# Kernel optimization log

Hardware: AMD Instinct MI355X
Metric: run time of the kernel (lower is better)

Reference implementation:

```python
import jax, jax.numpy as jnp
import numpy as np

N_NODES = 100000


def setup_inputs() -> dict:
    key = jax.random.key(0)
    ks = jax.random.split(key, 6)
    F_IN, F_CH, F_OUT = 64, 64, 64
    E = 1200000
    x = jax.random.normal(ks[0], (N_NODES, F_IN), dtype=jnp.float32)
    edge_index = jax.random.randint(ks[1], (2, E), 0, N_NODES, dtype=jnp.int64)
    # MLP params (PyTorch Linear default init scale ~ 1/sqrt(fan_in))
    s1 = 1.0 / np.sqrt(2 * F_IN)
    s2 = 1.0 / np.sqrt(F_CH)
    W1 = jax.random.uniform(ks[2], (2 * F_IN, F_CH), jnp.float32, -s1, s1)
    b1 = jax.random.uniform(ks[3], (F_CH,), jnp.float32, -s1, s1)
    W2 = jax.random.uniform(ks[4], (F_CH, F_OUT), jnp.float32, -s2, s2)
    b2 = jax.random.uniform(ks[5], (F_OUT,), jnp.float32, -s2, s2)
    return {"x": x, "edge_index": edge_index, "W1": W1, "b1": b1, "W2": W2, "b2": b2}


def reference(x, edge_index, W1, b1, W2, b2):
    # PyG EdgeConv with aggr='add': out_i = sum_j MLP(concat[x_i, x_j - x_i])
    src = edge_index[0]  # j (source / neighbor)
    dst = edge_index[1]  # i (target, aggregation index)
    x_i = x[dst]                     # [E, F]
    x_j = x[src]                     # [E, F]
    msg = jnp.concatenate([x_i, x_j - x_i], axis=-1)      # [E, 2F]
    h = jax.nn.relu(msg @ W1 + b1) @ W2 + b2               # [E, F_out]
    agg = jax.ops.segment_sum(h, dst, num_segments=N_NODES)  # [N, F_out]
    return jnp.tanh(agg)
```

## Files before the change

kernel.cpp:

```cpp
#include <hip/hip_runtime.h>
#include <math.h>


#define FDIM 64
#define BN 128
#define BSH 7
#define CAPB 2048
#define MAXB 1024
#define EPB 4096
#define XS_W 33
#define PRE_SMEM 24832

typedef unsigned int u32;
typedef unsigned short u16;
typedef _Float16 hf;

__device__ __forceinline__ float bf_lo(u32 u) {
    union { u32 i; float f; } c; c.i = u << 16; return c.f;
}
__device__ __forceinline__ float bf_hi(u32 u) {
    union { u32 i; float f; } c; c.i = u & 0xffff0000u; return c.f;
}
__device__ __forceinline__ u32 f2bf_rne(float f) {
    union { float f; u32 u; } c; c.f = f;
    u32 u = c.u;
    u += 0x7fffu + ((u >> 16) & 1u);
    return u >> 16;
}
__device__ __forceinline__ u32 f2h(float f) {
    union { u16 s; hf h; } c; c.h = (hf)f; return (u32)c.s;
}
__device__ __forceinline__ float h_lo(u32 u) {
    union { u16 s; hf h; } c; c.s = (u16)(u & 0xffffu); return (float)c.h;
}
__device__ __forceinline__ float h_hi(u32 u) {
    union { u16 s; hf h; } c; c.s = (u16)(u >> 16); return (float)c.h;
}

__global__ __launch_bounds__(256) void wprep_k(
    const float* __restrict__ W1, const float* __restrict__ W2,
    u32* __restrict__ Wchg, u32* __restrict__ W2hg)
{
    const int tid = threadIdx.x;
    for (int i = tid; i < 4096; i += 256) {
        int k = i >> 6, p = i & 63;
        u32 pk;
        if (p < 32) {
            int c = p * 2;
            float a0 = W1[k * 64 + c]     - W1[(64 + k) * 64 + c];
            float a1 = W1[k * 64 + c + 1] - W1[(64 + k) * 64 + c + 1];
            pk = f2h(a0) | (f2h(a1) << 16);
        } else {
            int c = (p - 32) * 2;
            pk = f2h(W1[(64 + k) * 64 + c]) | (f2h(W1[(64 + k) * 64 + c + 1]) << 16);
        }
        Wchg[i] = pk;
    }
    for (int i = tid; i < 2048; i += 256) {
        int k = i >> 5, c2 = i & 31;
        W2hg[i] = f2h(W2[k * 64 + c2 * 2]) | (f2h(W2[k * 64 + c2 * 2 + 1]) << 16);
    }
}

__global__ __launch_bounds__(256) void prep_k(
    const float* __restrict__ x, const u32* __restrict__ Wchg,
    const float* __restrict__ b1, u16* __restrict__ Ah,
    u16* __restrict__ Bmh, const int* __restrict__ ei,
    u32* __restrict__ slotB, int* __restrict__ gcnt,
    int N, int E, int NB, int nPre, int nBin)
{
    __shared__ __align__(16) char smem[PRE_SMEM];
    const int idx = blockIdx.x;
    const int tid = threadIdx.x;

    if ((idx % 6) == 5) {
        const int bb = idx / 6;
        if (bb >= nBin) return;
        int* histL = (int*)smem;
        int* gbase = histL + MAXB;
        const int e0 = bb * EPB;

        for (int j = tid; j < NB; j += 256) histL[j] = 0;
        __syncthreads();

        #pragma unroll
        for (int i = 0; i < EPB / 256; ++i) {
            int e = e0 + i * 256 + tid;
            if (e < E) {
                int d = ei[E + e];
                atomicAdd(&histL[d >> BSH], 1);
            }
        }
        __syncthreads();

        for (int j = tid; j < NB; j += 256) {
            int h = histL[j];
            gbase[j] = (h > 0) ? atomicAdd(&gcnt[j], h) : 0;
            histL[j] = 0;
        }
        __syncthreads();

        #pragma unroll
        for (int i = 0; i < EPB / 256; ++i) {
            int e = e0 + i * 256 + tid;
            if (e < E) {
                int s = ei[e];
                int d = ei[E + e];
                int b = d >> BSH;
                int pos = gbase[b] + atomicAdd(&histL[b], 1);
                if (pos < CAPB)
                    slotB[(size_t)b * CAPB + pos] =
                        ((u32)(d & (BN - 1)) << 20) | (u32)s;
            }
        }
        return;
    }

    const int pb = idx - idx / 6;
    if (pb >= nPre) return;
    u32 (*Wch)[64] = (u32(*)[64])smem;
    u32* xs = (u32*)(smem + 16384);

    const int node0 = pb * 64;

    {
        const uint4* Wg4 = (const uint4*)Wchg;
        #pragma unroll
        for (int it = 0; it < 4; ++it) {
            int i = it * 256 + tid;
            uint4 w = Wg4[i];
            *(uint4*)&Wch[i >> 4][(i & 15) * 4] = w;
        }
    }
    {
        const float4* X4 = (const float4*)x;
        #pragma unroll
        for (int it = 0; it < 4; ++it) {
            int i = it * 256 + tid;
            int n = i >> 4, k4 = i & 15;
            int gn = node0 + n;
            float4 v = make_float4(0.f, 0.f, 0.f, 0.f);
            if (gn < N) v = X4[(size_t)gn * 16 + k4];
            xs[n * XS_W + 2 * k4]     = f2h(v.x) | (f2h(v.y) << 16);
            xs[n * XS_W + 2 * k4 + 1] = f2h(v.z) | (f2h(v.w) << 16);
        }
    }
    __syncthreads();

    const int ng = tid & 15, cg = tid >> 4;
    const int n0 = ng * 4, c0 = cg * 8;
    const int wbase = (cg & 7) * 4 + ((cg >> 3) * 32);

    float acc[4][8];
    #pragma unroll
    for (int ci = 0; ci < 8; ++ci) {
        float init = b1[(c0 + ci) & 63];
        if (c0 >= 64) init = 0.f;
        #pragma unroll
        for (int ni = 0; ni < 4; ++ni) acc[ni][ci] = init;
    }

    #pragma unroll 4
    for (int kk = 0; kk < 32; ++kk) {
        u32 xv[4];
        #pragma unroll
        for (int ni = 0; ni < 4; ++ni) xv[ni] = xs[(n0 + ni) * XS_W + kk];
        uint4 w0 = *(const uint4*)&Wch[2 * kk][wbase];
        uint4 w1 = *(const uint4*)&Wch[2 * kk + 1][wbase];
        float ws0[8] = {h_lo(w0.x), h_hi(w0.x), h_lo(w0.y), h_hi(w0.y),
                        h_lo(w0.z), h_hi(w0.z), h_lo(w0.w), h_hi(w0.w)};
        float ws1[8] = {h_lo(w1.x), h_hi(w1.x), h_lo(w1.y), h_hi(w1.y),
                        h_lo(w1.z), h_hi(w1.z), h_lo(w1.w), h_hi(w1.w)};
        #pragma unroll
        for (int ni = 0; ni < 4; ++ni) {
            float xa = h_lo(xv[ni]);
            float xb = h_hi(xv[ni]);
            #pragma unroll
            for (int ci = 0; ci < 8; ++ci)
                acc[ni][ci] += xa * ws0[ci] + xb * ws1[ci];
        }
    }

    #pragma unroll
    for (int ni = 0; ni < 4; ++ni) {
        int n = node0 + n0 + ni;
        if (n >= N) break;
        if (c0 < 64) {
            uint4 pk;
            pk.x = f2h(acc[ni][0]) | (f2h(acc[ni][1]) << 16);
            pk.y = f2h(acc[ni][2]) | (f2h(acc[ni][3]) << 16);
            pk.z = f2h(acc[ni][4]) | (f2h(acc[ni][5]) << 16);
            pk.w = f2h(acc[ni][6]) | (f2h(acc[ni][7]) << 16);
            *(uint4*)&Ah[(size_t)n * 64 + c0] = pk;
        } else {
            uint4 pk;
            pk.x = f2bf_rne(acc[ni][0]) | (f2bf_rne(acc[ni][1]) << 16);
            pk.y = f2bf_rne(acc[ni][2]) | (f2bf_rne(acc[ni][3]) << 16);
            pk.z = f2bf_rne(acc[ni][4]) | (f2bf_rne(acc[ni][5]) << 16);
            pk.w = f2bf_rne(acc[ni][6]) | (f2bf_rne(acc[ni][7]) << 16);
            *(uint4*)&Bmh[(size_t)n * 64 + (c0 - 64)] = pk;
        }
    }
}

__device__ __forceinline__ float4 relu4add(float4 acc, float4 a, float4 b) {
    acc.x += fmaxf(a.x + b.x, 0.f);
    acc.y += fmaxf(a.y + b.y, 0.f);
    acc.z += fmaxf(a.z + b.z, 0.f);
    acc.w += fmaxf(a.w + b.w, 0.f);
    return acc;
}
__device__ __forceinline__ float4 relu4add_m(float4 acc, float4 a, float4 b, bool m) {
    acc.x += m ? fmaxf(a.x + b.x, 0.f) : 0.f;
    acc.y += m ? fmaxf(a.y + b.y, 0.f) : 0.f;
    acc.z += m ? fmaxf(a.z + b.z, 0.f) : 0.f;
    acc.w += m ? fmaxf(a.w + b.w, 0.f) : 0.f;
    return acc;
}
__device__ __forceinline__ float4 bf4(uint2 u) {
    return make_float4(bf_lo(u.x), bf_hi(u.x), bf_lo(u.y), bf_hi(u.y));
}

__global__ __launch_bounds__(256) void fused_agg(
    const u16* __restrict__ Ah, const u16* __restrict__ Bmh,
    const u32* __restrict__ slotB, const int* __restrict__ gcnt,
    const u32* __restrict__ W2hg, const float* __restrict__ b2,
    float* __restrict__ out, int N)
{
    __shared__ __align__(16) u32 W2h[64][34];
    __shared__ __align__(16) u32 pool[BN * 17 * 2];
    __shared__ u32 csrS[CAPB];
    __shared__ int histL[BN];
    __shared__ int rowO[BN + 1];
    __shared__ int ofs[BN];
    __shared__ float b2s[64];

    u32* eStage = pool;
    uint2* aggTb = (uint2*)pool;

    const int tid = threadIdx.x;
    const int b = blockIdx.x;
    const int node0 = b * BN;
    const int cntB = min(gcnt[b], CAPB);

    {
        const uint4* Wg4 = (const uint4*)W2hg;
        #pragma unroll
        for (int it = 0; it < 2; ++it) {
            int i = it * 256 + tid;
            uint4 w = Wg4[i];
            *(uint4*)&W2h[i >> 3][(i & 7) * 4] = w;
        }
    }
    if (tid < 64) b2s[tid] = b2[tid];
    if (tid < BN) histL[tid] = 0;
    __syncthreads();

    for (int i = tid; i < cntB; i += 256) {
        u32 e = slotB[(size_t)b * CAPB + i];
        eStage[i] = e;
        atomicAdd(&histL[e >> 20], 1);
    }
    __syncthreads();

    if (tid < 64) {
        int l = tid;
        int h0 = histL[2 * l], h1 = histL[2 * l + 1];
        int s = h0 + h1, inc = s;
        #pragma unroll
        for (int off = 1; off < 64; off <<= 1) {
            int t = __shfl_up(inc, off);
            if (l >= off) inc += t;
        }
        int base = inc - s;
        rowO[2 * l] = base; rowO[2 * l + 1] = base + h0;
        ofs[2 * l] = base;  ofs[2 * l + 1] = base + h0;
        if (l == 63) rowO[BN] = inc;
    }
    __syncthreads();

    for (int i = tid; i < cntB; i += 256) {
        u32 e = eStage[i];
        int pos = atomicAdd(&ofs[e >> 20], 1);
        csrS[pos] = e & 0xFFFFFu;
    }
    __syncthreads();

    {
        const int q = tid & 15, ng = tid >> 4;
        const uint2* __restrict__ B2 = (const uint2*)Bmh;
        const uint2* __restrict__ A2 = (const uint2*)Ah;
        #pragma unroll
        for (int h = 0; h < 8; ++h) {
            int nl = ng + h * 16;
            int gn = node0 + nl;
            int start = rowO[nl];
            int d = (gn < N) ? (rowO[nl + 1] - start) : 0;
            float4 a = make_float4(0.f, 0.f, 0.f, 0.f);
            if (gn < N) {
                uint2 ua = A2[(size_t)gn * 16 + q];
                a = make_float4(h_lo(ua.x), h_hi(ua.x), h_lo(ua.y), h_hi(ua.y));
            }
            float4 acc = make_float4(0.f, 0.f, 0.f, 0.f);

            int j = 0;
            for (; j + 8 <= d; j += 8) {
                int ss[8];
                uint2 bb[8];
                #pragma unroll
                for (int t = 0; t < 8; ++t) ss[t] = csrS[start + j + t];
                #pragma unroll
                for (int t = 0; t < 8; ++t) bb[t] = B2[(size_t)ss[t] * 16 + q];
                #pragma unroll
                for (int t = 0; t < 8; ++t) acc = relu4add(acc, a, bf4(bb[t]));
            }
            if (j < d) {
                int ss[8];
                uint2 bb[8];
                #pragma unroll
                for (int t = 0; t < 8; ++t) ss[t] = csrS[start + min(j + t, d - 1)];
                #pragma unroll
                for (int t = 0; t < 8; ++t) bb[t] = B2[(size_t)ss[t] * 16 + q];
                acc = relu4add(acc, a, bf4(bb[0]));
                #pragma unroll
                for (int t = 1; t < 8; ++t)
                    acc = relu4add_m(acc, a, bf4(bb[t]), j + t < d);
            }
            uint2 pk;
            pk.x = f2h(acc.x) | (f2h(acc.y) << 16);
            pk.y = f2h(acc.z) | (f2h(acc.w) << 16);
            aggTb[nl * 17 + q] = pk;
        }
    }
    __syncthreads();

    {
        const int cg = tid & 15, g0 = tid >> 4;
        const int c0 = cg * 4;
        #pragma unroll
        for (int h = 0; h < 2; ++h) {
            int g = g0 + h * 16;
            int nb0 = g * 4;
            float o[4][4];
            #pragma unroll
            for (int ni = 0; ni < 4; ++ni) {
                float dg = (float)(rowO[nb0 + ni + 1] - rowO[nb0 + ni]);
                #pragma unroll
                for (int ci = 0; ci < 4; ++ci) o[ni][ci] = dg * b2s[c0 + ci];
            }
            #pragma unroll 2
            for (int kc = 0; kc < 16; ++kc) {
                uint2 u0 = aggTb[(nb0 + 0) * 17 + kc];
                uint2 u1 = aggTb[(nb0 + 1) * 17 + kc];
                uint2 u2 = aggTb[(nb0 + 2) * 17 + kc];
                uint2 u3 = aggTb[(nb0 + 3) * 17 + kc];
                #pragma unroll
                for (int kk = 0; kk < 4; ++kk) {
                    uint2 w2p = *(const uint2*)&W2h[kc * 4 + kk][cg * 2];
                    float wv[4] = {h_lo(w2p.x), h_hi(w2p.x), h_lo(w2p.y), h_hi(w2p.y)};
                    float a0 = (kk < 2) ? ((kk == 0) ? h_lo(u0.x) : h_hi(u0.x))
                                        : ((kk == 2) ? h_lo(u0.y) : h_hi(u0.y));
                    float a1 = (kk < 2) ? ((kk == 0) ? h_lo(u1.x) : h_hi(u1.x))
                                        : ((kk == 2) ? h_lo(u1.y) : h_hi(u1.y));
                    float a2 = (kk < 2) ? ((kk == 0) ? h_lo(u2.x) : h_hi(u2.x))
                                        : ((kk == 2) ? h_lo(u2.y) : h_hi(u2.y));
                    float a3 = (kk < 2) ? ((kk == 0) ? h_lo(u3.x) : h_hi(u3.x))
                                        : ((kk == 2) ? h_lo(u3.y) : h_hi(u3.y));
                    #pragma unroll
                    for (int ci = 0; ci < 4; ++ci) {
                        o[0][ci] += a0 * wv[ci];
                        o[1][ci] += a1 * wv[ci];
                        o[2][ci] += a2 * wv[ci];
                        o[3][ci] += a3 * wv[ci];
                    }
                }
            }
            #pragma unroll
            for (int ni = 0; ni < 4; ++ni) {
                int gn = node0 + nb0 + ni;
                if (gn < N) {
                    float4 r = make_float4(tanhf(o[ni][0]), tanhf(o[ni][1]),
                                           tanhf(o[ni][2]), tanhf(o[ni][3]));
                    ((float4*)out)[(size_t)gn * 16 + cg] = r;
                }
            }
        }
    }
}

extern "C" void kernel_launch(void* const* d_in, const int* in_sizes, int n_in,
                              void* d_out, int out_size, void* d_ws, size_t ws_size,
                              hipStream_t stream)
{
    const float* x  = (const float*)d_in[0];
    const int*   ei = (const int*)d_in[1];
    const float* W1 = (const float*)d_in[2];
    const float* b1 = (const float*)d_in[3];
    const float* W2 = (const float*)d_in[4];
    const float* b2 = (const float*)d_in[5];
    float* out = (float*)d_out;

    const int N = in_sizes[0] / FDIM;
    const int E = in_sizes[1] / 2;
    const int NB = (N + BN - 1) / BN;

    u16*   Ah    = (u16*)d_ws;
    u16*   Bmh   = Ah + (size_t)N * FDIM;
    u32*   slotB = (u32*)(Bmh + (size_t)N * FDIM);
    u32*   Wchg  = slotB + (size_t)NB * CAPB;
    u32*   W2hg  = Wchg + 4096;
    int*   gcnt  = (int*)(W2hg + 2048);

    hipMemsetAsync(gcnt, 0, (size_t)NB * sizeof(int), stream);

    wprep_k<<<1, 256, 0, stream>>>(W1, W2, Wchg, W2hg);

    const int nPre = (N + 63) / 64;
    const int nBin = (E + EPB - 1) / EPB;
    int T = (nPre * 6 + 4) / 5;
    while (T - T / 6 < nPre) ++T;
    if (T < 6 * nBin) T = 6 * nBin;

    prep_k<<<T, 256, 0, stream>>>(x, Wchg, b1, Ah, Bmh, ei, slotB, gcnt,
                                  N, E, NB, nPre, nBin);
    fused_agg<<<NB, 256, 0, stream>>>(Ah, Bmh, slotB, gcnt, W2hg, b2, out, N);
}
```

Before: 195.3 us.

## Fold gcnt memset into wprep, rebalance binning blocks, use packed-float ReLU accumulate

Zeroes the bin counters inside the weight-prep kernel so the separate memset launch goes away. Halves edges per binning block and changes the interleave from 1-in-6 to 1-in-4 blocks, giving more parallel binning work. Rewrites the aggregation inner loop on two-wide float vectors so the compiler can emit packed FP32 add and max. It also adds a 4-edge step and shrinks the masked tail from 8 to 4 loads to cut wasted gathers. The smaller per-block edge count means more blocks contend on the global bin-count atomics.

```diff
diff --git a/kernel.cpp b/kernel.cpp
--- a/kernel.cpp
+++ b/kernel.cpp
@@ -7,13 +7,14 @@
 #define BSH 7
 #define CAPB 2048
 #define MAXB 1024
-#define EPB 4096
+#define EPB 2048
 #define XS_W 33
 #define PRE_SMEM 24832
 
 typedef unsigned int u32;
 typedef unsigned short u16;
 typedef _Float16 hf;
+typedef float f2 __attribute__((ext_vector_type(2)));
 
 __device__ __forceinline__ float bf_lo(u32 u) {
     union { u32 i; float f; } c; c.i = u << 16; return c.f;
@@ -39,7 +40,8 @@
 
 __global__ __launch_bounds__(256) void wprep_k(
     const float* __restrict__ W1, const float* __restrict__ W2,
-    u32* __restrict__ Wchg, u32* __restrict__ W2hg)
+    u32* __restrict__ Wchg, u32* __restrict__ W2hg,
+    int* __restrict__ gcnt, int NB)
 {
     const int tid = threadIdx.x;
     for (int i = tid; i < 4096; i += 256) {
@@ -60,6 +62,7 @@
         int k = i >> 5, c2 = i & 31;
         W2hg[i] = f2h(W2[k * 64 + c2 * 2]) | (f2h(W2[k * 64 + c2 * 2 + 1]) << 16);
     }
+    for (int i = tid; i < NB; i += 256) gcnt[i] = 0;
 }
 
 __global__ __launch_bounds__(256) void prep_k(
@@ -73,8 +76,8 @@
     const int idx = blockIdx.x;
     const int tid = threadIdx.x;
 
-    if ((idx % 6) == 5) {
-        const int bb = idx / 6;
+    if ((idx & 3) == 3) {
+        const int bb = idx >> 2;
         if (bb >= nBin) return;
         int* histL = (int*)smem;
         int* gbase = histL + MAXB;
@@ -116,7 +119,7 @@
         return;
     }
 
-    const int pb = idx - idx / 6;
+    const int pb = idx - (idx >> 2);
     if (pb >= nPre) return;
     u32 (*Wch)[64] = (u32(*)[64])smem;
     u32* xs = (u32*)(smem + 16384);
@@ -203,22 +206,27 @@
     }
 }
 
-__device__ __forceinline__ float4 relu4add(float4 acc, float4 a, float4 b) {
-    acc.x += fmaxf(a.x + b.x, 0.f);
-    acc.y += fmaxf(a.y + b.y, 0.f);
-    acc.z += fmaxf(a.z + b.z, 0.f);
-    acc.w += fmaxf(a.w + b.w, 0.f);
-    return acc;
-}
-__device__ __forceinline__ float4 relu4add_m(float4 acc, float4 a, float4 b, bool m) {
-    acc.x += m ? fmaxf(a.x + b.x, 0.f) : 0.f;
-    acc.y += m ? fmaxf(a.y + b.y, 0.f) : 0.f;
-    acc.z += m ? fmaxf(a.z + b.z, 0.f) : 0.f;
-    acc.w += m ? fmaxf(a.w + b.w, 0.f) : 0.f;
-    return acc;
-}
-__device__ __forceinline__ float4 bf4(uint2 u) {
-    return make_float4(bf_lo(u.x), bf_hi(u.x), bf_lo(u.y), bf_hi(u.y));
+__device__ __forceinline__ void radd2(f2& acc0, f2& acc1, f2 a0, f2 a1, uint2 b) {
+    f2 bv0, bv1;
+    bv0.x = bf_lo(b.x); bv0.y = bf_hi(b.x);
+    bv1.x = bf_lo(b.y); bv1.y = bf_hi(b.y);
+    f2 z = {0.f, 0.f};
+    f2 t0 = a0 + bv0, t1 = a1 + bv1;
+    t0 = __builtin_elementwise_max(t0, z);
+    t1 = __builtin_elementwise_max(t1, z);
+    acc0 = acc0 + t0;
+    acc1 = acc1 + t1;
+}
+__device__ __forceinline__ void radd2_m(f2& acc0, f2& acc1, f2 a0, f2 a1,
+                                        uint2 b, bool m) {
+    f2 bv0, bv1;
+    bv0.x = bf_lo(b.x); bv0.y = bf_hi(b.x);
+    bv1.x = bf_lo(b.y); bv1.y = bf_hi(b.y);
+    f2 z = {0.f, 0.f};
+    f2 t0 = a0 + bv0, t1 = a1 + bv1;
+    t0 = __builtin_elementwise_max(t0, z);
+    t1 = __builtin_elementwise_max(t1, z);
+    if (m) { acc0 = acc0 + t0; acc1 = acc1 + t1; }
 }
 
 __global__ __launch_bounds__(256) void fused_agg(
@@ -296,12 +304,13 @@
             int gn = node0 + nl;
             int start = rowO[nl];
             int d = (gn < N) ? (rowO[nl + 1] - start) : 0;
-            float4 a = make_float4(0.f, 0.f, 0.f, 0.f);
+            f2 a0 = {0.f, 0.f}, a1 = {0.f, 0.f};
             if (gn < N) {
                 uint2 ua = A2[(size_t)gn * 16 + q];
-                a = make_float4(h_lo(ua.x), h_hi(ua.x), h_lo(ua.y), h_hi(ua.y));
-            }
-            float4 acc = make_float4(0.f, 0.f, 0.f, 0.f);
+                a0.x = h_lo(ua.x); a0.y = h_hi(ua.x);
+                a1.x = h_lo(ua.y); a1.y = h_hi(ua.y);
+            }
+            f2 acc0 = {0.f, 0.f}, acc1 = {0.f, 0.f};
 
             int j = 0;
             for (; j + 8 <= d; j += 8) {
@@ -312,23 +321,34 @@
                 #pragma unroll
                 for (int t = 0; t < 8; ++t) bb[t] = B2[(size_t)ss[t] * 16 + q];
                 #pragma unroll
-                for (int t = 0; t < 8; ++t) acc = relu4add(acc, a, bf4(bb[t]));
+                for (int t = 0; t < 8; ++t) radd2(acc0, acc1, a0, a1, bb[t]);
+            }
+            if (j + 4 <= d) {
+                int ss[4];
+                uint2 bb[4];
+                #pragma unroll
+                for (int t = 0; t < 4; ++t) ss[t] = csrS[start + j + t];
+                #pragma unroll
+                for (int t = 0; t < 4; ++t) bb[t] = B2[(size_t)ss[t] * 16 + q];
+                #pragma unroll
+                for (int t = 0; t < 4; ++t) radd2(acc0, acc1, a0, a1, bb[t]);
+                j += 4;
             }
             if (j < d) {
-                int ss[8];
-                uint2 bb[8];
-                #pragma unroll
-                for (int t = 0; t < 8; ++t) ss[t] = csrS[start + min(j + t, d - 1)];
-                #pragma unroll
-                for (int t = 0; t < 8; ++t) bb[t] = B2[(size_t)ss[t] * 16 + q];
-                acc = relu4add(acc, a, bf4(bb[0]));
-                #pragma unroll
-                for (int t = 1; t < 8; ++t)
-                    acc = relu4add_m(acc, a, bf4(bb[t]), j + t < d);
+                int ss[4];
+                uint2 bb[4];
+                #pragma unroll
+                for (int t = 0; t < 4; ++t) ss[t] = csrS[start + min(j + t, d - 1)];
+                #pragma unroll
+                for (int t = 0; t < 4; ++t) bb[t] = B2[(size_t)ss[t] * 16 + q];
+                radd2(acc0, acc1, a0, a1, bb[0]);
+                #pragma unroll
+                for (int t = 1; t < 4; ++t)
+                    radd2_m(acc0, acc1, a0, a1, bb[t], j + t < d);
             }
             uint2 pk;
-            pk.x = f2h(acc.x) | (f2h(acc.y) << 16);
-            pk.y = f2h(acc.z) | (f2h(acc.w) << 16);
+            pk.x = f2h(acc0.x) | (f2h(acc0.y) << 16);
+            pk.y = f2h(acc1.x) | (f2h(acc1.y) << 16);
             aggTb[nl * 17 + q] = pk;
         }
     }
@@ -411,15 +431,13 @@
     u32*   W2hg  = Wchg + 4096;
     int*   gcnt  = (int*)(W2hg + 2048);
 
-    hipMemsetAsync(gcnt, 0, (size_t)NB * sizeof(int), stream);
-
-    wprep_k<<<1, 256, 0, stream>>>(W1, W2, Wchg, W2hg);
+    wprep_k<<<1, 256, 0, stream>>>(W1, W2, Wchg, W2hg, gcnt, NB);
 
     const int nPre = (N + 63) / 64;
     const int nBin = (E + EPB - 1) / EPB;
-    int T = (nPre * 6 + 4) / 5;
-    while (T - T / 6 < nPre) ++T;
-    if (T < 6 * nBin) T = 6 * nBin;
+    int T = (nPre * 4 + 2) / 3;
+    while (T - (T >> 2) < nPre) ++T;
+    if ((T >> 2) < nBin) T = 4 * nBin;
 
     prep_k<<<T, 256, 0, stream>>>(x, Wchg, b1, Ah, Bmh, ei, slotB, gcnt,
                                   N, E, NB, nPre, nBin);
```

Measured after the change: 202.9 us. 3.9% more time.
